# Kernel optimization log

Hardware: AMD Instinct MI355X
Metric: run time of the kernel (lower is better)

Reference implementation:

```python
import jax, jax.numpy as jnp
import numpy as np

N_HEAD = 16
N_EMBD = 1024
B, T = 4, 2048


def setup_inputs() -> dict:
    key = jax.random.key(0)
    ks = jax.random.split(key, 5)
    s_in = 1.0 / np.sqrt(N_EMBD)
    return {
        "x": jax.random.normal(ks[0], (B, T, N_EMBD), dtype=jnp.float32),
        "W_qkv": jax.random.normal(ks[1], (N_EMBD, 3 * N_EMBD), dtype=jnp.float32) * s_in,
        "b_qkv": jnp.zeros((3 * N_EMBD,), dtype=jnp.float32),
        "W_proj": jax.random.normal(ks[2], (N_EMBD, N_EMBD), dtype=jnp.float32) * s_in,
        "b_proj": jnp.zeros((N_EMBD,), dtype=jnp.float32),
    }


def reference(x, W_qkv, b_qkv, W_proj, b_proj):
    Bb, Tt, C = x.shape
    H = N_HEAD
    hd = C // H  # head dim
    qkv = x @ W_qkv + b_qkv                      # [B,T,3C]
    q, k, v = jnp.split(qkv, 3, axis=-1)
    # [B,H,T,hd]
    q = q.reshape(Bb, Tt, H, hd).transpose(0, 2, 1, 3)
    k = k.reshape(Bb, Tt, H, hd).transpose(0, 2, 1, 3)
    v = v.reshape(Bb, Tt, H, hd).transpose(0, 2, 1, 3)
    scale = 1.0 / np.sqrt(hd).astype(np.float32)
    att = jnp.einsum("bhqd,bhkd->bhqk", q, k) * scale
    causal = jnp.tril(jnp.ones((Tt, Tt), dtype=bool))
    att = jnp.where(causal, att, jnp.float32(-jnp.inf))
    att = jax.nn.softmax(att, axis=-1)
    y = jnp.einsum("bhqk,bhkd->bhqd", att, v)    # [B,H,T,hd]
    y = y.transpose(0, 2, 1, 3).reshape(Bb, Tt, C)
    return y @ W_proj + b_proj
```

## Files before the change

kernel.cpp:

```cpp
#include <hip/hip_runtime.h>
#include <hip/hip_bf16.h>
#include <math.h>

typedef unsigned short u16;
typedef _Float16 f16_t;
typedef f16_t f16x8 __attribute__((ext_vector_type(8)));
typedef float f32x4 __attribute__((ext_vector_type(4)));

#define N_HEADC 16
#define C_EMBD  1024
#define B_SZ    4
#define T_SEQ   2048
#define HD      64
#define M_TOT   (B_SZ * T_SEQ)

#define BM 128
#define BN 256
#define BK 32
#define NT (C_EMBD / BK)
#define A_T (BM * BK)
#define B_T (BN * BK)

#define SWZ_CHUNK(l) ((((l) & 3) ^ (((l) >> 3) & 3)) * 8)

__device__ __forceinline__ u16 f2h(float f) {
    f16_t h = (f16_t)f;
    return __builtin_bit_cast(u16, h);
}
__device__ __forceinline__ unsigned pkf16(float a, float b) {
    unsigned lo = f2h(a), hi = f2h(b);
    return lo | (hi << 16);
}
__device__ __forceinline__ float fexp2(float x) {
#if __has_builtin(__builtin_amdgcn_exp2f)
    return __builtin_amdgcn_exp2f(x);
#else
    return exp2f(x);
#endif
}
__device__ __forceinline__ void gl_lds16(const u16* g, u16* l) {
    __builtin_amdgcn_global_load_lds(
        (const __attribute__((address_space(1))) unsigned int*)g,
        (__attribute__((address_space(3))) unsigned int*)l,
        16, 0, 0);
}

__global__ __launch_bounds__(256) void prep(const float* __restrict__ x,
                                            const float* __restrict__ Wqkv,
                                            const float* __restrict__ Wproj,
                                            u16* __restrict__ xh,
                                            u16* __restrict__ WqkvT,
                                            u16* __restrict__ WprojT) {
    __shared__ float tile[32][33];
    int bid = blockIdx.x, tid = threadIdx.x;
    if (bid < 8192) {
        int i = bid * 1024 + tid * 4;
        float4 v = *(const float4*)(x + i);
        ushort4 o;
        o.x = f2h(v.x); o.y = f2h(v.y); o.z = f2h(v.z); o.w = f2h(v.w);
        *(ushort4*)(xh + i) = o;
        return;
    }
    const float* in; u16* outp; int N, bx, by;
    if (bid < 8192 + 3072) {
        int b2 = bid - 8192; bx = b2 % 96; by = b2 / 96;
        in = Wqkv; outp = WqkvT; N = 3 * C_EMBD;
    } else {
        int b2 = bid - 11264; bx = b2 % 32; by = b2 / 32;
        in = Wproj; outp = WprojT; N = C_EMBD;
    }
    int tx = tid & 31, ty = tid >> 5;
    int n0 = bx * 32, k0 = by * 32;
    for (int i = ty; i < 32; i += 8)
        tile[i][tx] = in[(size_t)(k0 + i) * N + n0 + tx];
    __syncthreads();
    for (int i = ty; i < 32; i += 8)
        outp[(size_t)(n0 + i) * C_EMBD + k0 + tx] = f2h(tile[tx][i]);
}

#define GEMM_PROLOGUE(Ap, BTp)                                                  \
    int m0 = blockIdx.y * BM;                                                   \
    int n0 = blockIdx.x * BN;                                                   \
    int tid = threadIdx.x;                                                      \
    int w = tid >> 6, lane = tid & 63;                                          \
    int wm = w >> 2, wn = w & 3;                                                \
    int quad = lane >> 4, rl = lane & 15;                                       \
    int srow = lane >> 2, sko = SWZ_CHUNK(lane);                                \
    int kx = (rl >> 1) & 3;                       \
    int qx = (quad ^ kx) * 8;                                                   \
    f32x4 acc[4][4];                                                            \
    _Pragma("unroll")                                                           \
    for (int i = 0; i < 4; ++i)                                                 \
        _Pragma("unroll")                                                       \
        for (int j = 0; j < 4; ++j)                                             \
            acc[i][j] = f32x4{0.f, 0.f, 0.f, 0.f};                              \
    const u16* gA  = Ap  + (size_t)(m0 + w * 16 + srow) * C_EMBD + sko;         \
    const u16* gB0 = BTp + (size_t)(n0 + w * 16 + srow) * C_EMBD + sko;         \
    const u16* gB1 = gB0 + (size_t)128 * C_EMBD;                                \
    u16* lA = sA + w * 512;                                                     \
    u16* lB = sB + w * 512;                                                     \
                                        \
    gl_lds16(gA,      lA);                                                      \
    gl_lds16(gB0,     lB);                                                      \
    gl_lds16(gB1,     lB + 128 * BK);                                           \
    gl_lds16(gA + BK,  lA + A_T);                                               \
    gl_lds16(gB0 + BK, lB + B_T);                                               \
    gl_lds16(gB1 + BK, lB + B_T + 128 * BK);                                    \
    gA += 2 * BK; gB0 += 2 * BK; gB1 += 2 * BK;                                 \
    int bufR = 0, bufS = 2;                                                     \
    for (int t = 0; t < NT; ++t) {                                              \
        if (t == NT - 1) asm volatile("s_waitcnt vmcnt(0)" ::: "memory");       \
        else             asm volatile("s_waitcnt vmcnt(3)" ::: "memory");       \
        asm volatile("s_barrier" ::: "memory");                                 \
        const u16* pA = sA + bufR * A_T + (wm * 64) * BK;                       \
        const u16* pB = sB + bufR * B_T + (wn * 64) * BK;                       \
        f16x8 af[4], bfr[4];                                                    \
        _Pragma("unroll")                                                       \
        for (int i = 0; i < 4; ++i)                                             \
            af[i] = *(const f16x8*)&pA[(i * 16 + rl) * BK + qx];                \
        _Pragma("unroll")                                                       \
        for (int j = 0; j < 4; ++j)                                             \
            bfr[j] = *(const f16x8*)&pB[(j * 16 + rl) * BK + qx];               \
        if (t + 2 < NT) {                                                       \
            u16* dA = sA + bufS * A_T + w * 512;                                \
            u16* dB = sB + bufS * B_T + w * 512;                                \
            gl_lds16(gA,  dA);                                                  \
            gl_lds16(gB0, dB);                                                  \
            gl_lds16(gB1, dB + 128 * BK);                                       \
            gA += BK; gB0 += BK; gB1 += BK;                                     \
        }                                                                       \
        __builtin_amdgcn_s_setprio(1);                                          \
        _Pragma("unroll")                                                       \
        for (int i = 0; i < 4; ++i)                                             \
            _Pragma("unroll")                                                   \
            for (int j = 0; j < 4; ++j)                                         \
                acc[i][j] = __builtin_amdgcn_mfma_f32_16x16x32_f16(             \
                    af[i], bfr[j], acc[i][j], 0, 0, 0);                         \
        __builtin_amdgcn_s_setprio(0);                                          \
        bufR = bufR == 2 ? 0 : bufR + 1;                                        \
        bufS = bufS == 2 ? 0 : bufS + 1;                                        \
    }

__global__ __launch_bounds__(512) void gemm_qkv(const u16* __restrict__ A,
                                                const u16* __restrict__ BT,
                                                const float* __restrict__ bias,
                                                u16* __restrict__ qQ,
                                                u16* __restrict__ qK,
                                                u16* __restrict__ qVt) {
    __shared__ __align__(16) u16 sA[3 * A_T];
    __shared__ __align__(16) u16 sB[3 * B_T];
    GEMM_PROLOGUE(A, BT)

    const float QSC = 0.18033688011112042f;
    int p = n0 >> 10;
    if (p < 2) {
        u16* dst = p == 0 ? qQ : qK;
        float sc = p == 0 ? QSC : 1.0f;
        #pragma unroll
        for (int j = 0; j < 4; ++j) {
            int n = n0 + wn * 64 + j * 16 + rl;
            float bv = bias[n];
            int cch = n & 1023;
            int h = cch >> 6, d = cch & 63;
            #pragma unroll
            for (int i = 0; i < 4; ++i) {
                int mbase = m0 + wm * 64 + i * 16 + quad * 4;
                int bb = mbase >> 11, t0 = mbase & 2047;
                size_t thbase = ((size_t)bb * N_HEADC + h) * T_SEQ;
                #pragma unroll
                for (int r = 0; r < 4; ++r)
                    dst[(thbase + t0 + r) * HD + d] = f2h((acc[i][j][r] + bv) * sc);
            }
        }
    } else {
        u16 (*tr)[136] = (u16 (*)[136])sA;
        int bb = m0 >> 11, t0g = m0 & 2047;
        #pragma unroll
        for (int c = 0; c < 4; ++c) {
            __syncthreads();
            if (wn == c) {
                #pragma unroll
                for (int j = 0; j < 4; ++j) {
                    int rowr = j * 16 + rl;
                    float bv = bias[n0 + c * 64 + rowr];
                    #pragma unroll
                    for (int i = 0; i < 4; ++i) {
                        int mm = wm * 64 + i * 16 + quad * 4;
                        *(unsigned*)&tr[rowr][mm]     = pkf16(acc[i][j][0] + bv, acc[i][j][1] + bv);
                        *(unsigned*)&tr[rowr][mm + 2] = pkf16(acc[i][j][2] + bv, acc[i][j][3] + bv);
                    }
                }
            }
            __syncthreads();
            #pragma unroll
            for (int s = 0; s < 2; ++s) {
                int task = s * 512 + tid;
                int nn = task >> 4, seg = task & 15;
                int ch = (n0 & 1023) + c * 64 + nn;
                int h = ch >> 6, d = ch & 63;
                size_t di = (((size_t)bb * N_HEADC + h) * HD + d) * T_SEQ + t0g + seg * 8;
                *(uint4*)&qVt[di] = *(const uint4*)&tr[nn][seg * 8];
            }
        }
    }
}

__global__ __launch_bounds__(512) void gemm_proj(const u16* __restrict__ A,
                                                 const u16* __restrict__ BT,
                                                 const float* __restrict__ bias,
                                                 float* __restrict__ out) {
    __shared__ __align__(16) u16 sA[3 * A_T];
    __shared__ __align__(16) u16 sB[3 * B_T];
    GEMM_PROLOGUE(A, BT)

    #pragma unroll
    for (int i = 0; i < 4; ++i) {
        int mbase = m0 + wm * 64 + i * 16 + quad * 4;
        #pragma unroll
        for (int j = 0; j < 4; ++j) {
            int n = n0 + wn * 64 + j * 16 + rl;
            float bv = bias[n];
            #pragma unroll
            for (int r = 0; r < 4; ++r)
                out[(size_t)(mbase + r) * C_EMBD + n] = acc[i][j][r] + bv;
        }
    }
}

__global__ __launch_bounds__(512) void attn_mfma(const u16* __restrict__ Qg,
                                                 const u16* __restrict__ Kg,
                                                 const u16* __restrict__ Vtg,
                                                 u16* __restrict__ yh) {
    int bid = blockIdx.x;
    int a  = bid >> 6;
    int g  = bid & 63;
    int j  = a < 4 ? a : 11 - a;
    int h = g & 15, b = g >> 4;
    const size_t hs = (size_t)T_SEQ * HD;
    const u16* Qp  = Qg  + ((size_t)b * N_HEADC + h) * hs;
    const u16* Kp  = Kg  + ((size_t)b * N_HEADC + h) * hs;
    const u16* Vtp = Vtg + ((size_t)b * N_HEADC + h) * hs;

    __shared__ __align__(16) u16 sK[2][2][64][32];
    __shared__ __align__(16) u16 sVt[2][2][64][32];
    __shared__ __align__(16) u16 sP[8][32][72];

    int tid = threadIdx.x;
    int lane = tid & 63, w = tid >> 6;
    int quad = lane >> 4, rl = lane & 15;
    int kx = (rl >> 1) & 3;
    int qx = (quad ^ kx) * 8;
    u16* sPw = &sP[w][0][0];
    int srow = lane >> 2;
    int sch = SWZ_CHUNK(lane);
    const f32x4 mneg = {-4.f, -4.f, -4.f, -4.f};

    int qt  = (w < 4) ? (15 - j) : j;
    int q0w = qt * 128 + (w & 3) * 32;
    int nkt = 2 * (15 - j) + 2;

    const u16* gp[2];
    u16* ld0[2]; u16* ld1[2];
    int gstep;
    if (w < 4) {
        gstep = 64 * HD;
        int half = (w >> 1) & 1, rbase = (w & 1) * 32;
        #pragma unroll
        for (int c = 0; c < 2; ++c) {
            int r = rbase + c * 16;
            gp[c]  = Kp + (size_t)(r + srow) * HD + half * 32 + sch;
            ld0[c] = &sK[0][half][r][0];
            ld1[c] = &sK[1][half][r][0];
        }
    } else {
        gstep = 64;
        int v = w - 4;
        int half = (v >> 1) & 1, rbase = (v & 1) * 32;
        #pragma unroll
        for (int c = 0; c < 2; ++c) {
            int r = rbase + c * 16;
            gp[c]  = Vtp + (size_t)(r + srow) * T_SEQ + half * 32 + sch;
            ld0[c] = &sVt[0][half][r][0];
            ld1[c] = &sVt[1][half][r][0];
        }
    }

    f16x8 qf[2][2];
    #pragma unroll
    for (int nt = 0; nt < 2; ++nt)
        #pragma unroll
        for (int ks = 0; ks < 2; ++ks)
            qf[nt][ks] = *(const f16x8*)&Qp[(size_t)(q0w + nt * 16 + rl) * HD + ks * 32 + quad * 8];

    f32x4 O[2][4];
    #pragma unroll
    for (int mi = 0; mi < 2; ++mi)
        #pragma unroll
        for (int nd = 0; nd < 4; ++nd)
            O[mi][nd] = f32x4{0.f, 0.f, 0.f, 0.f};
    float l_[2] = {0.f, 0.f};

    gl_lds16(gp[0], ld0[0]);
    gl_lds16(gp[1], ld0[1]);

    for (int kt = 0; kt < nkt; ++kt) {
        __syncthreads();
        int buf = kt & 1;
        int k0 = kt * 64;
        if (kt + 1 < nkt) {
            u16* const* ldn = ((kt + 1) & 1) ? ld1 : ld0;
            #pragma unroll
            for (int c = 0; c < 2; ++c) {
                gp[c] += gstep;
                gl_lds16(gp[c], ldn[c]);
            }
        }
        if (k0 > q0w + 31) continue;

        f32x4 st[4][2];
        #pragma unroll
        for (int mt = 0; mt < 4; ++mt) {
            f16x8 ak0 = *(const f16x8*)&sK[buf][0][mt * 16 + rl][qx];
            f16x8 ak1 = *(const f16x8*)&sK[buf][1][mt * 16 + rl][qx];
            #pragma unroll
            for (int nt = 0; nt < 2; ++nt) {
                f32x4 t = __builtin_amdgcn_mfma_f32_16x16x32_f16(ak0, qf[nt][0], mneg, 0, 0, 0);
                st[mt][nt] = __builtin_amdgcn_mfma_f32_16x16x32_f16(ak1, qf[nt][1], t, 0, 0, 0);
            }
        }

        if (k0 + 63 > q0w) {
            #pragma unroll
            for (int mt = 0; mt < 4; ++mt)
                #pragma unroll
                for (int nt = 0; nt < 2; ++nt)
                    #pragma unroll
                    for (int r = 0; r < 4; ++r) {
                        int kpos = k0 + mt * 16 + quad * 4 + r;
                        int q = q0w + nt * 16 + rl;
                        if (kpos > q) st[mt][nt][r] = -INFINITY;
                    }
        }

        #pragma unroll
        for (int nt = 0; nt < 2; ++nt) {
            float lsum = 0.f;
            #pragma unroll
            for (int mt = 0; mt < 4; ++mt) {
                float p0 = fexp2(st[mt][nt][0]);
                float p1 = fexp2(st[mt][nt][1]);
                float p2 = fexp2(st[mt][nt][2]);
                float p3 = fexp2(st[mt][nt][3]);
                lsum += (p0 + p1) + (p2 + p3);
                *(uint2*)&sPw[(nt * 16 + rl) * 72 + mt * 16 + quad * 4] =
                    make_uint2(pkf16(p0, p1), pkf16(p2, p3));
            }
            l_[nt] += lsum;
        }

        #pragma unroll
        for (int ks = 0; ks < 2; ++ks) {
            f16x8 ap0 = *(const f16x8*)&sPw[(0 * 16 + rl) * 72 + ks * 32 + quad * 8];
            f16x8 ap1 = *(const f16x8*)&sPw[(1 * 16 + rl) * 72 + ks * 32 + quad * 8];
            #pragma unroll
            for (int nd = 0; nd < 4; ++nd) {
                f16x8 bv = *(const f16x8*)&sVt[buf][ks][nd * 16 + rl][qx];
                O[0][nd] = __builtin_amdgcn_mfma_f32_16x16x32_f16(ap0, bv, O[0][nd], 0, 0, 0);
                O[1][nd] = __builtin_amdgcn_mfma_f32_16x16x32_f16(ap1, bv, O[1][nd], 0, 0, 0);
            }
        }
    }

    #pragma unroll
    for (int nt = 0; nt < 2; ++nt) {
        l_[nt] += __shfl_xor(l_[nt], 16);
        l_[nt] += __shfl_xor(l_[nt], 32);
    }
    float linv[2] = {1.f / l_[0], 1.f / l_[1]};
    int idxq = quad * 4;
    #pragma unroll
    for (int mi = 0; mi < 2; ++mi)
        #pragma unroll
        for (int r = 0; r < 4; ++r) {
            float li = __shfl(linv[mi], idxq + r);
            int qg = q0w + mi * 16 + quad * 4 + r;
            size_t base = ((size_t)b * T_SEQ + qg) * C_EMBD + h * HD;
            #pragma unroll
            for (int nd = 0; nd < 4; ++nd)
                yh[base + nd * 16 + rl] = f2h(O[mi][nd][r] * li);
        }
}

extern "C" void kernel_launch(void* const* d_in, const int* in_sizes, int n_in,
                              void* d_out, int out_size, void* d_ws, size_t ws_size,
                              hipStream_t stream) {
    const float* x     = (const float*)d_in[0];
    const float* Wqkv  = (const float*)d_in[1];
    const float* bqkv  = (const float*)d_in[2];
    const float* Wproj = (const float*)d_in[3];
    const float* bproj = (const float*)d_in[4];
    float* out = (float*)d_out;

    char* ws = (char*)d_ws;
    u16* xh     = (u16*)(ws);
    u16* WqkvT  = (u16*)(ws + (size_t)16 * 1024 * 1024);
    u16* WprojT = (u16*)(ws + (size_t)22 * 1024 * 1024);
    u16* qQ     = (u16*)(ws + (size_t)24 * 1024 * 1024);
    u16* qK     = (u16*)(ws + (size_t)40 * 1024 * 1024);
    u16* qVt    = (u16*)(ws + (size_t)56 * 1024 * 1024);
    u16* yh     = (u16*)(ws + (size_t)72 * 1024 * 1024);

    prep<<<dim3(12288), dim3(256), 0, stream>>>(x, Wqkv, Wproj, xh, WqkvT, WprojT);
    gemm_qkv<<<dim3(3 * C_EMBD / BN, M_TOT / BM), dim3(512), 0, stream>>>(
        xh, WqkvT, bqkv, qQ, qK, qVt);
    attn_mfma<<<dim3(512), dim3(512), 0, stream>>>(
        qQ, qK, qVt, yh);
    gemm_proj<<<dim3(C_EMBD / BN, M_TOT / BM), dim3(512), 0, stream>>>(
        yh, WprojT, bproj, out);
}
```

Before: 236.9 us.

## Split GEMM k-step into two barrier-separated phases and stage Q/K epilogue via LDS

New measurement: 237.5 us. No clear change (+0.3%).

```diff
diff --git a/kernel.cpp b/kernel.cpp
--- a/kernel.cpp
+++ b/kernel.cpp
@@ -20,6 +20,7 @@
 #define NT (C_EMBD / BK)
 #define A_T (BM * BK)
 #define B_T (BN * BK)
+#define SMEM_U16 (3 * A_T + 3 * B_T)
 
 #define SWZ_CHUNK(l) ((((l) & 3) ^ (((l) >> 3) & 3)) * 8)
 
@@ -79,6 +80,8 @@
 }
 
 #define GEMM_PROLOGUE(Ap, BTp)                                                  \
+    u16* sA = smem;                                                             \
+    u16* sB = smem + 3 * A_T;                                                   \
     int m0 = blockIdx.y * BM;                                                   \
     int n0 = blockIdx.x * BN;                                                   \
     int tid = threadIdx.x;                                                      \
@@ -118,22 +121,34 @@
         _Pragma("unroll")                                                       \
         for (int i = 0; i < 4; ++i)                                             \
             af[i] = *(const f16x8*)&pA[(i * 16 + rl) * BK + qx];                \
+        bfr[0] = *(const f16x8*)&pB[(0 * 16 + rl) * BK + qx];                   \
+        bfr[1] = *(const f16x8*)&pB[(1 * 16 + rl) * BK + qx];                   \
+        if (t + 2 < NT) {                                                       \
+            gl_lds16(gA,  sA + bufS * A_T + w * 512);                           \
+            gl_lds16(gB0, sB + bufS * B_T + w * 512);                           \
+        }                                                                       \
+        asm volatile("s_barrier" ::: "memory");                                 \
+        __builtin_amdgcn_s_setprio(1);                                          \
         _Pragma("unroll")                                                       \
-        for (int j = 0; j < 4; ++j)                                             \
-            bfr[j] = *(const f16x8*)&pB[(j * 16 + rl) * BK + qx];               \
+        for (int j = 0; j < 2; ++j)                                             \
+            _Pragma("unroll")                                                   \
+            for (int i = 0; i < 4; ++i)                                         \
+                acc[i][j] = __builtin_amdgcn_mfma_f32_16x16x32_f16(             \
+                    af[i], bfr[j], acc[i][j], 0, 0, 0);                         \
+        __builtin_amdgcn_s_setprio(0);                                          \
+        asm volatile("s_barrier" ::: "memory");                                 \
+        bfr[2] = *(const f16x8*)&pB[(2 * 16 + rl) * BK + qx];                   \
+        bfr[3] = *(const f16x8*)&pB[(3 * 16 + rl) * BK + qx];                   \
         if (t + 2 < NT) {                                                       \
-            u16* dA = sA + bufS * A_T + w * 512;                                \
-            u16* dB = sB + bufS * B_T + w * 512;                                \
-            gl_lds16(gA,  dA);                                                  \
-            gl_lds16(gB0, dB);                                                  \
-            gl_lds16(gB1, dB + 128 * BK);                                       \
+            gl_lds16(gB1, sB + bufS * B_T + 128 * BK + w * 512);                \
             gA += BK; gB0 += BK; gB1 += BK;                                     \
         }                                                                       \
+        asm volatile("s_barrier" ::: "memory");                                 \
         __builtin_amdgcn_s_setprio(1);                                          \
         _Pragma("unroll")                                                       \
-        for (int i = 0; i < 4; ++i)                                             \
+        for (int j = 2; j < 4; ++j)                                             \
             _Pragma("unroll")                                                   \
-            for (int j = 0; j < 4; ++j)                                         \
+            for (int i = 0; i < 4; ++i)                                         \
                 acc[i][j] = __builtin_amdgcn_mfma_f32_16x16x32_f16(             \
                     af[i], bfr[j], acc[i][j], 0, 0, 0);                         \
         __builtin_amdgcn_s_setprio(0);                                          \
@@ -147,37 +162,46 @@
                                                 u16* __restrict__ qQ,
                                                 u16* __restrict__ qK,
                                                 u16* __restrict__ qVt) {
-    __shared__ __align__(16) u16 sA[3 * A_T];
-    __shared__ __align__(16) u16 sB[3 * B_T];
+    __shared__ __align__(16) u16 smem[SMEM_U16];
     GEMM_PROLOGUE(A, BT)
+
+    __syncthreads();
 
     const float QSC = 0.18033688011112042f;
     int p = n0 >> 10;
     if (p < 2) {
         u16* dst = p == 0 ? qQ : qK;
         float sc = p == 0 ? QSC : 1.0f;
+        u16* myep = smem + w * 4608;
         #pragma unroll
         for (int j = 0; j < 4; ++j) {
-            int n = n0 + wn * 64 + j * 16 + rl;
-            float bv = bias[n];
-            int cch = n & 1023;
-            int h = cch >> 6, d = cch & 63;
+            float bv = bias[n0 + wn * 64 + j * 16 + rl];
             #pragma unroll
             for (int i = 0; i < 4; ++i) {
-                int mbase = m0 + wm * 64 + i * 16 + quad * 4;
-                int bb = mbase >> 11, t0 = mbase & 2047;
-                size_t thbase = ((size_t)bb * N_HEADC + h) * T_SEQ;
+                int row = i * 16 + quad * 4;
+                int col = (j * 16 + rl) ^ ((quad >> 1) << 4);
                 #pragma unroll
                 for (int r = 0; r < 4; ++r)
-                    dst[(thbase + t0 + r) * HD + d] = f2h((acc[i][j][r] + bv) * sc);
-            }
+                    myep[(row + r) * 72 + col] = f2h((acc[i][j][r] + bv) * sc);
+            }
+        }
+        int hch = ((n0 & 1023) + wn * 64) >> 6;
+        size_t rowbase = ((size_t)(m0 >> 11) * N_HEADC + hch) * T_SEQ
+                       + (m0 & 2047) + wm * 64;
+        #pragma unroll
+        for (int it = 0; it < 8; ++it) {
+            int idx = it * 64 + lane;
+            int row = idx >> 3, seg = idx & 7;
+            int col = (seg * 8) ^ (((row >> 3) & 1) << 4);
+            *(uint4*)&dst[(rowbase + row) * HD + seg * 8] =
+                *(const uint4*)&myep[row * 72 + col];
         }
     } else {
-        u16 (*tr)[136] = (u16 (*)[136])sA;
+        u16 (*tr)[136] = (u16 (*)[136])smem;
         int bb = m0 >> 11, t0g = m0 & 2047;
         #pragma unroll
         for (int c = 0; c < 4; ++c) {
-            __syncthreads();
+            if (c) __syncthreads();
             if (wn == c) {
                 #pragma unroll
                 for (int j = 0; j < 4; ++j) {
@@ -209,8 +233,7 @@
                                                  const u16* __restrict__ BT,
                                                  const float* __restrict__ bias,
                                                  float* __restrict__ out) {
-    __shared__ __align__(16) u16 sA[3 * A_T];
-    __shared__ __align__(16) u16 sB[3 * B_T];
+    __shared__ __align__(16) u16 smem[SMEM_U16];
     GEMM_PROLOGUE(A, BT)
 
     #pragma unroll
```

## Split GEMM mainloops into interleaved phases and stage Q/K epilogue via LDS

Applied to the files above, without the earlier changes.

After: 237.3 us. No clear change (+0.2%).

```diff
diff --git a/kernel.cpp b/kernel.cpp
--- a/kernel.cpp
+++ b/kernel.cpp
@@ -78,106 +78,128 @@
         outp[(size_t)(n0 + i) * C_EMBD + k0 + tx] = f2h(tile[tx][i]);
 }
 
-#define GEMM_PROLOGUE(Ap, BTp)                                                  \
-    int m0 = blockIdx.y * BM;                                                   \
-    int n0 = blockIdx.x * BN;                                                   \
-    int tid = threadIdx.x;                                                      \
-    int w = tid >> 6, lane = tid & 63;                                          \
-    int wm = w >> 2, wn = w & 3;                                                \
-    int quad = lane >> 4, rl = lane & 15;                                       \
-    int srow = lane >> 2, sko = SWZ_CHUNK(lane);                                \
-    int kx = (rl >> 1) & 3;                       \
-    int qx = (quad ^ kx) * 8;                                                   \
-    f32x4 acc[4][4];                                                            \
-    _Pragma("unroll")                                                           \
-    for (int i = 0; i < 4; ++i)                                                 \
-        _Pragma("unroll")                                                       \
-        for (int j = 0; j < 4; ++j)                                             \
-            acc[i][j] = f32x4{0.f, 0.f, 0.f, 0.f};                              \
-    const u16* gA  = Ap  + (size_t)(m0 + w * 16 + srow) * C_EMBD + sko;         \
-    const u16* gB0 = BTp + (size_t)(n0 + w * 16 + srow) * C_EMBD + sko;         \
-    const u16* gB1 = gB0 + (size_t)128 * C_EMBD;                                \
-    u16* lA = sA + w * 512;                                                     \
-    u16* lB = sB + w * 512;                                                     \
-                                        \
-    gl_lds16(gA,      lA);                                                      \
-    gl_lds16(gB0,     lB);                                                      \
-    gl_lds16(gB1,     lB + 128 * BK);                                           \
-    gl_lds16(gA + BK,  lA + A_T);                                               \
-    gl_lds16(gB0 + BK, lB + B_T);                                               \
-    gl_lds16(gB1 + BK, lB + B_T + 128 * BK);                                    \
-    gA += 2 * BK; gB0 += 2 * BK; gB1 += 2 * BK;                                 \
-    int bufR = 0, bufS = 2;                                                     \
-    for (int t = 0; t < NT; ++t) {                                              \
-        if (t == NT - 1) asm volatile("s_waitcnt vmcnt(0)" ::: "memory");       \
-        else             asm volatile("s_waitcnt vmcnt(3)" ::: "memory");       \
-        asm volatile("s_barrier" ::: "memory");                                 \
-        const u16* pA = sA + bufR * A_T + (wm * 64) * BK;                       \
-        const u16* pB = sB + bufR * B_T + (wn * 64) * BK;                       \
-        f16x8 af[4], bfr[4];                                                    \
-        _Pragma("unroll")                                                       \
-        for (int i = 0; i < 4; ++i)                                             \
-            af[i] = *(const f16x8*)&pA[(i * 16 + rl) * BK + qx];                \
-        _Pragma("unroll")                                                       \
-        for (int j = 0; j < 4; ++j)                                             \
-            bfr[j] = *(const f16x8*)&pB[(j * 16 + rl) * BK + qx];               \
-        if (t + 2 < NT) {                                                       \
-            u16* dA = sA + bufS * A_T + w * 512;                                \
-            u16* dB = sB + bufS * B_T + w * 512;                                \
-            gl_lds16(gA,  dA);                                                  \
-            gl_lds16(gB0, dB);                                                  \
-            gl_lds16(gB1, dB + 128 * BK);                                       \
-            gA += BK; gB0 += BK; gB1 += BK;                                     \
-        }                                                                       \
-        __builtin_amdgcn_s_setprio(1);                                          \
-        _Pragma("unroll")                                                       \
-        for (int i = 0; i < 4; ++i)                                             \
-            _Pragma("unroll")                                                   \
-            for (int j = 0; j < 4; ++j)                                         \
-                acc[i][j] = __builtin_amdgcn_mfma_f32_16x16x32_f16(             \
-                    af[i], bfr[j], acc[i][j], 0, 0, 0);                         \
-        __builtin_amdgcn_s_setprio(0);                                          \
-        bufR = bufR == 2 ? 0 : bufR + 1;                                        \
-        bufS = bufS == 2 ? 0 : bufS + 1;                                        \
-    }
-
 __global__ __launch_bounds__(512) void gemm_qkv(const u16* __restrict__ A,
                                                 const u16* __restrict__ BT,
                                                 const float* __restrict__ bias,
                                                 u16* __restrict__ qQ,
                                                 u16* __restrict__ qK,
                                                 u16* __restrict__ qVt) {
-    __shared__ __align__(16) u16 sA[3 * A_T];
-    __shared__ __align__(16) u16 sB[3 * B_T];
-    GEMM_PROLOGUE(A, BT)
+    __shared__ __align__(16) u16 smem[2 * A_T + 2 * B_T];
+    u16* sA = smem;
+    u16* sB = smem + 2 * A_T;
+    int m0 = blockIdx.y * BM;
+    int n0 = blockIdx.x * BN;
+    int tid = threadIdx.x;
+    int w = tid >> 6, lane = tid & 63;
+    int wm = w >> 2, wn = w & 3;
+    int quad = lane >> 4, rl = lane & 15;
+    int srow = lane >> 2, sko = SWZ_CHUNK(lane);
+    int kx = (rl >> 1) & 3;
+    int qx = (quad ^ kx) * 8;
+
+    f32x4 acc[4][4];
+    #pragma unroll
+    for (int i = 0; i < 4; ++i)
+        #pragma unroll
+        for (int j = 0; j < 4; ++j)
+            acc[i][j] = f32x4{0.f, 0.f, 0.f, 0.f};
+
+    const u16* gA  = A  + (size_t)(m0 + w * 16 + srow) * C_EMBD + sko;
+    const u16* gB0 = BT + (size_t)(n0 + w * 16 + srow) * C_EMBD + sko;
+    const u16* gB1 = gB0 + (size_t)128 * C_EMBD;
+
+    gl_lds16(gA,  sA + w * 512);
+    gl_lds16(gB0, sB + w * 512);
+    gl_lds16(gB1, sB + 128 * BK + w * 512);
+    gA += BK; gB0 += BK; gB1 += BK;
+
+    for (int t = 0; t < NT; ++t) {
+        asm volatile("s_waitcnt vmcnt(0)" ::: "memory");
+        asm volatile("s_barrier" ::: "memory");
+        const u16* pA = sA + (t & 1) * A_T + (wm * 64) * BK;
+        const u16* pB = sB + (t & 1) * B_T + (wn * 64) * BK;
+        f16x8 af[4], bfr[4];
+        #pragma unroll
+        for (int i = 0; i < 4; ++i)
+            af[i] = *(const f16x8*)&pA[(i * 16 + rl) * BK + qx];
+        bfr[0] = *(const f16x8*)&pB[(0 * 16 + rl) * BK + qx];
+        bfr[1] = *(const f16x8*)&pB[(1 * 16 + rl) * BK + qx];
+        if (t + 1 < NT) {
+            int ns = (t + 1) & 1;
+            gl_lds16(gA,  sA + ns * A_T + w * 512);
+            gl_lds16(gB0, sB + ns * B_T + w * 512);
+        }
+        asm volatile("s_barrier" ::: "memory");
+        __builtin_amdgcn_s_setprio(1);
+        #pragma unroll
+        for (int j = 0; j < 2; ++j)
+            #pragma unroll
+            for (int i = 0; i < 4; ++i)
+                acc[i][j] = __builtin_amdgcn_mfma_f32_16x16x32_f16(
+                    af[i], bfr[j], acc[i][j], 0, 0, 0);
+        __builtin_amdgcn_s_setprio(0);
+        asm volatile("s_barrier" ::: "memory");
+        bfr[2] = *(const f16x8*)&pB[(2 * 16 + rl) * BK + qx];
+        bfr[3] = *(const f16x8*)&pB[(3 * 16 + rl) * BK + qx];
+        if (t + 1 < NT) {
+            gl_lds16(gB1, sB + ((t + 1) & 1) * B_T + 128 * BK + w * 512);
+            gA += BK; gB0 += BK; gB1 += BK;
+        }
+        asm volatile("s_barrier" ::: "memory");
+        __builtin_amdgcn_s_setprio(1);
+        #pragma unroll
+        for (int j = 2; j < 4; ++j)
+            #pragma unroll
+            for (int i = 0; i < 4; ++i)
+                acc[i][j] = __builtin_amdgcn_mfma_f32_16x16x32_f16(
+                    af[i], bfr[j], acc[i][j], 0, 0, 0);
+        __builtin_amdgcn_s_setprio(0);
+    }
+
+    __syncthreads();
 
     const float QSC = 0.18033688011112042f;
     int p = n0 >> 10;
     if (p < 2) {
+        u16* ep = smem;
         u16* dst = p == 0 ? qQ : qK;
         float sc = p == 0 ? QSC : 1.0f;
-        #pragma unroll
-        for (int j = 0; j < 4; ++j) {
-            int n = n0 + wn * 64 + j * 16 + rl;
-            float bv = bias[n];
-            int cch = n & 1023;
-            int h = cch >> 6, d = cch & 63;
-            #pragma unroll
-            for (int i = 0; i < 4; ++i) {
-                int mbase = m0 + wm * 64 + i * 16 + quad * 4;
-                int bb = mbase >> 11, t0 = mbase & 2047;
-                size_t thbase = ((size_t)bb * N_HEADC + h) * T_SEQ;
+        int hbase = (n0 & 1023) >> 6;
+        #pragma unroll
+        for (int c = 0; c < 4; ++c) {
+            if (c) __syncthreads();
+            if (wn == c) {
                 #pragma unroll
-                for (int r = 0; r < 4; ++r)
-                    dst[(thbase + t0 + r) * HD + d] = f2h((acc[i][j][r] + bv) * sc);
+                for (int j = 0; j < 4; ++j) {
+                    float bv = bias[n0 + c * 64 + j * 16 + rl];
+                    int col = (j * 16 + rl) ^ ((quad >> 1) << 4);
+                    #pragma unroll
+                    for (int i = 0; i < 4; ++i) {
+                        int row = wm * 64 + i * 16 + quad * 4;
+                        #pragma unroll
+                        for (int r = 0; r < 4; ++r)
+                            ep[(row + r) * 72 + col] = f2h((acc[i][j][r] + bv) * sc);
+                    }
+                }
+            }
+            __syncthreads();
+            size_t rowbase = ((size_t)(m0 >> 11) * N_HEADC + hbase + c) * T_SEQ
+                           + (m0 & 2047);
+            #pragma unroll
+            for (int s = 0; s < 2; ++s) {
+                int task = s * 512 + tid;
+                int row = task >> 3, seg = task & 7;
+                int colr = (seg * 8) ^ (((row >> 3) & 1) << 4);
+                *(uint4*)&dst[(rowbase + row) * HD + seg * 8] =
+                    *(const uint4*)&ep[row * 72 + colr];
             }
         }
     } else {
-        u16 (*tr)[136] = (u16 (*)[136])sA;
+        u16 (*tr)[136] = (u16 (*)[136])smem;
         int bb = m0 >> 11, t0g = m0 & 2047;
         #pragma unroll
         for (int c = 0; c < 4; ++c) {
-            __syncthreads();
+            if (c) __syncthreads();
             if (wn == c) {
                 #pragma unroll
                 for (int j = 0; j < 4; ++j) {
@@ -209,9 +231,81 @@
                                                  const u16* __restrict__ BT,
                                                  const float* __restrict__ bias,
                                                  float* __restrict__ out) {
-    __shared__ __align__(16) u16 sA[3 * A_T];
-    __shared__ __align__(16) u16 sB[3 * B_T];
-    GEMM_PROLOGUE(A, BT)
+    __shared__ __align__(16) u16 smem[3 * A_T + 3 * B_T];
+    u16* sA = smem;
+    u16* sB = smem + 3 * A_T;
+    int m0 = blockIdx.y * BM;
+    int n0 = blockIdx.x * BN;
+    int tid = threadIdx.x;
+    int w = tid >> 6, lane = tid & 63;
+    int wm = w >> 2, wn = w & 3;
+    int quad = lane >> 4, rl = lane & 15;
+    int srow = lane >> 2, sko = SWZ_CHUNK(lane);
+    int kx = (rl >> 1) & 3;
+    int qx = (quad ^ kx) * 8;
+
+    f32x4 acc[4][4];
+    #pragma unroll
+    for (int i = 0; i < 4; ++i)
+        #pragma unroll
+        for (int j = 0; j < 4; ++j)
+            acc[i][j] = f32x4{0.f, 0.f, 0.f, 0.f};
+
+    const u16* gA  = A  + (size_t)(m0 + w * 16 + srow) * C_EMBD + sko;
+    const u16* gB0 = BT + (size_t)(n0 + w * 16 + srow) * C_EMBD + sko;
+    const u16* gB1 = gB0 + (size_t)128 * C_EMBD;
+    gl_lds16(gA,       sA + w * 512);
+    gl_lds16(gB0,      sB + w * 512);
+    gl_lds16(gB1,      sB + 128 * BK + w * 512);
+    gl_lds16(gA + BK,  sA + A_T + w * 512);
+    gl_lds16(gB0 + BK, sB + B_T + w * 512);
+    gl_lds16(gB1 + BK, sB + B_T + 128 * BK + w * 512);
+    gA += 2 * BK; gB0 += 2 * BK; gB1 += 2 * BK;
+    int bufR = 0, bufS = 2;
+    for (int t = 0; t < NT; ++t) {
+        if (t == NT - 1) asm volatile("s_waitcnt vmcnt(0)" ::: "memory");
+        else             asm volatile("s_waitcnt vmcnt(3)" ::: "memory");
+        asm volatile("s_barrier" ::: "memory");
+        const u16* pA = sA + bufR * A_T + (wm * 64) * BK;
+        const u16* pB = sB + bufR * B_T + (wn * 64) * BK;
+        f16x8 af[4], bfr[4];
+        #pragma unroll
+        for (int i = 0; i < 4; ++i)
+            af[i] = *(const f16x8*)&pA[(i * 16 + rl) * BK + qx];
+        bfr[0] = *(const f16x8*)&pB[(0 * 16 + rl) * BK + qx];
+        bfr[1] = *(const f16x8*)&pB[(1 * 16 + rl) * BK + qx];
+        if (t + 2 < NT) {
+            gl_lds16(gA,  sA + bufS * A_T + w * 512);
+            gl_lds16(gB0, sB + bufS * B_T + w * 512);
+        }
+        asm volatile("s_barrier" ::: "memory");
+        __builtin_amdgcn_s_setprio(1);
+        #pragma unroll
+        for (int j = 0; j < 2; ++j)
+            #pragma unroll
+            for (int i = 0; i < 4; ++i)
+                acc[i][j] = __builtin_amdgcn_mfma_f32_16x16x32_f16(
+                    af[i], bfr[j], acc[i][j], 0, 0, 0);
+        __builtin_amdgcn_s_setprio(0);
+        asm volatile("s_barrier" ::: "memory");
+        bfr[2] = *(const f16x8*)&pB[(2 * 16 + rl) * BK + qx];
+        bfr[3] = *(const f16x8*)&pB[(3 * 16 + rl) * BK + qx];
+        if (t + 2 < NT) {
+            gl_lds16(gB1, sB + bufS * B_T + 128 * BK + w * 512);
+            gA += BK; gB0 += BK; gB1 += BK;
+        }
+        asm volatile("s_barrier" ::: "memory");
+        __builtin_amdgcn_s_setprio(1);
+        #pragma unroll
+        for (int j = 2; j < 4; ++j)
+            #pragma unroll
+            for (int i = 0; i < 4; ++i)
+                acc[i][j] = __builtin_amdgcn_mfma_f32_16x16x32_f16(
+                    af[i], bfr[j], acc[i][j], 0, 0, 0);
+        __builtin_amdgcn_s_setprio(0);
+        bufR = bufR == 2 ? 0 : bufR + 1;
+        bufS = bufS == 2 ? 0 : bufS + 1;
+    }
 
     #pragma unroll
     for (int i = 0; i < 4; ++i) {
```
